# Performance work log

Hardware: AMD Instinct MI355X
Metric: run time of the kernel (lower is better)

The kernel has to match this reference:

```python
import jax, jax.numpy as jnp
import numpy as np

D_IN = 1024
D_OUT = 1024
NUM_HEADS = 16
D_HEAD = D_OUT // NUM_HEADS


def setup_inputs() -> dict:
    key = jax.random.key(0)
    ks = jax.random.split(key, 6)
    s = 0.02
    x = jax.random.normal(ks[0], (2, 2048, D_IN), dtype=jnp.float32)
    Wq = jax.random.normal(ks[1], (D_IN, D_OUT), dtype=jnp.float32) * s
    Wk = jax.random.normal(ks[2], (D_IN, D_OUT), dtype=jnp.float32) * s
    Wv = jax.random.normal(ks[3], (D_IN, D_OUT), dtype=jnp.float32) * s
    Wo = jax.random.normal(ks[4], (D_OUT, D_OUT), dtype=jnp.float32) * s
    bo = jnp.zeros((D_OUT,), dtype=jnp.float32)
    return {"x": x, "Wq": Wq, "Wk": Wk, "Wv": Wv, "Wo": Wo, "bo": bo}


def reference(x, Wq, Wk, Wv, Wo, bo):
    bs, S, _ = x.shape
    # QKV projections -> [b, h, s, d]
    def split_heads(t):
        return t.reshape(bs, S, NUM_HEADS, D_HEAD).transpose(0, 2, 1, 3)
    q = split_heads(x @ Wq)
    k = split_heads(x @ Wk)
    v = split_heads(x @ Wv)
    # scores [b, h, s, s], causal mask, scaled softmax
    scores = jnp.einsum("bhqd,bhkd->bhqk", q, k)
    causal = jnp.tril(jnp.ones((S, S), dtype=bool))
    scores = jnp.where(causal, scores, -jnp.inf)
    attn = jax.nn.softmax(scores / jnp.sqrt(jnp.float32(D_HEAD)), axis=-1)
    # dropout rate is 0.0 -> identity
    ctx = jnp.einsum("bhqk,bhkd->bhqd", attn, v)
    ctx = ctx.transpose(0, 2, 1, 3).reshape(bs, S, D_OUT)
    return ctx @ Wo + bo
```

## Files before the change

kernel.cpp:

```cpp
#include <hip/hip_runtime.h>
#include <math.h>

namespace {

constexpr int S   = 2048;
constexpr int D   = 1024;
constexpr int H   = 16;
constexpr int DH  = 64;
constexpr int B   = 2;
constexpr int M   = B * S;

typedef __attribute__((ext_vector_type(8)))  short bf16x8;
typedef __attribute__((ext_vector_type(4)))  float f32x4;
typedef __attribute__((ext_vector_type(16))) float f32x16;

__device__ __forceinline__ unsigned short f2bf(float f) {
    unsigned u = __builtin_bit_cast(unsigned, f);
    u += 0x7fffu + ((u >> 16) & 1u);
    return (unsigned short)(u >> 16);
}

__device__ __forceinline__ unsigned cvt_pk_bf16(float lo, float hi) {
    unsigned r;
    asm("v_cvt_pk_bf16_f32 %0, %1, %2" : "=v"(r) : "v"(lo), "v"(hi));
    return r;
}

__device__ __forceinline__ void gload16(const void* g, void* l) {
    __builtin_amdgcn_global_load_lds(
        (const __attribute__((address_space(1))) void*)g,
        (__attribute__((address_space(3))) void*)l, 16, 0, 0);
}

__global__ __launch_bounds__(256) void convert_x(
    const float* __restrict__ x, unsigned short* __restrict__ xb)
{
    const int i = (blockIdx.x * 256 + threadIdx.x) * 8;
    float4 a = *(const float4*)&x[i];
    float4 b = *(const float4*)&x[i + 4];
    ushort4 lo, hi;
    lo.x = f2bf(a.x); lo.y = f2bf(a.y); lo.z = f2bf(a.z); lo.w = f2bf(a.w);
    hi.x = f2bf(b.x); hi.y = f2bf(b.y); hi.z = f2bf(b.z); hi.w = f2bf(b.w);
    *(ushort4*)&xb[i]     = lo;
    *(ushort4*)&xb[i + 4] = hi;
}

__global__ __launch_bounds__(64) void convert_w(
    const float* __restrict__ Wq, const float* __restrict__ Wk,
    const float* __restrict__ Wv, const float* __restrict__ Wo,
    unsigned short* __restrict__ Wt)
{
    const int mat = blockIdx.z;
    const float* W = (mat == 0) ? Wq : (mat == 1) ? Wk : (mat == 2) ? Wv : Wo;
    const int n  = blockIdx.y * 64 + threadIdx.x;
    const int k0 = blockIdx.x * 8;
    ushort4 u0, u1;
    u0.x = f2bf(W[(size_t)(k0 + 0) * D + n]);
    u0.y = f2bf(W[(size_t)(k0 + 1) * D + n]);
    u0.z = f2bf(W[(size_t)(k0 + 2) * D + n]);
    u0.w = f2bf(W[(size_t)(k0 + 3) * D + n]);
    u1.x = f2bf(W[(size_t)(k0 + 4) * D + n]);
    u1.y = f2bf(W[(size_t)(k0 + 5) * D + n]);
    u1.z = f2bf(W[(size_t)(k0 + 6) * D + n]);
    u1.w = f2bf(W[(size_t)(k0 + 7) * D + n]);
    unsigned short* o = Wt + (size_t)mat * D * D + (size_t)n * D + k0;
    *(ushort4*)&o[0] = u0;
    *(ushort4*)&o[4] = u1;
}

__global__ __launch_bounds__(256) void gemm_qkv(
    const unsigned short* __restrict__ xb, const unsigned short* __restrict__ Wt,
    unsigned short* __restrict__ Qb, unsigned short* __restrict__ Kb,
    unsigned short* __restrict__ Vt)
{
    __shared__ unsigned short As[128 * 32];
    __shared__ unsigned short Bs[128 * 32];

    const int tid = threadIdx.x;
    const int l  = tid & 63;
    const int w  = tid >> 6;
    const int lr = l & 15;
    const int g  = l >> 4;
    const int wr = w >> 1, wc = w & 1;

    const int bm  = blockIdx.y;
    const int bnl = blockIdx.x;
    const int mat = bnl >> 3;
    const int n0  = (bnl & 7) * 128;
    const int m0  = bm * 128;
    const unsigned short* Bp = Wt + (size_t)mat * D * D;

    const int lrow = l >> 2;
    const int lcol = (l & 3) * 8;

    f32x4 acc[4][4];
    #pragma unroll
    for (int i = 0; i < 4; ++i)
        #pragma unroll
        for (int j = 0; j < 4; ++j) acc[i][j] = (f32x4){0.f, 0.f, 0.f, 0.f};

    for (int k0 = 0; k0 < D; k0 += 32) {
        #pragma unroll
        for (int p = 0; p < 2; ++p) {
            const int c = w * 2 + p;
            gload16(&xb[(size_t)(m0 + c * 16 + lrow) * D + k0 + lcol], &As[c * 512]);
            gload16(&Bp[(size_t)(n0 + c * 16 + lrow) * D + k0 + lcol], &Bs[c * 512]);
        }
        __syncthreads();
        bf16x8 af[4], bfr[4];
        #pragma unroll
        for (int i = 0; i < 4; ++i) {
            af[i]  = *(const bf16x8*)&As[(wr * 64 + i * 16 + lr) * 32 + g * 8];
            bfr[i] = *(const bf16x8*)&Bs[(wc * 64 + i * 16 + lr) * 32 + g * 8];
        }
        #pragma unroll
        for (int mi = 0; mi < 4; ++mi)
            #pragma unroll
            for (int ni = 0; ni < 4; ++ni)
                acc[mi][ni] = __builtin_amdgcn_mfma_f32_16x16x32_bf16(
                    af[mi], bfr[ni], acc[mi][ni], 0, 0, 0);
        __syncthreads();
    }

    const int b      = m0 >> 11;
    const int s_base = (m0 & (S - 1)) + wr * 64;
    if (mat == 2) {
        #pragma unroll
        for (int ni = 0; ni < 4; ++ni) {
            const int n  = n0 + wc * 64 + ni * 16 + lr;
            const int bh = b * H + (n >> 6);
            unsigned short* vp = Vt + ((size_t)bh * DH + (n & 63)) * S;
            #pragma unroll
            for (int mi = 0; mi < 4; ++mi) {
                const int s0 = s_base + mi * 16 + g * 4;
                ushort4 u;
                u.x = f2bf(acc[mi][ni][0]); u.y = f2bf(acc[mi][ni][1]);
                u.z = f2bf(acc[mi][ni][2]); u.w = f2bf(acc[mi][ni][3]);
                *(ushort4*)&vp[s0] = u;
            }
        }
    } else {
        unsigned short* Op = (mat == 0) ? Qb : Kb;
        #pragma unroll
        for (int mi = 0; mi < 4; ++mi)
            #pragma unroll
            for (int r = 0; r < 4; ++r) {
                const int s = s_base + mi * 16 + g * 4 + r;
                #pragma unroll
                for (int ni = 0; ni < 4; ++ni) {
                    const int n  = n0 + wc * 64 + ni * 16 + lr;
                    const int bh = b * H + (n >> 6);
                    Op[((size_t)bh * S + s) * DH + (n & 63)] = f2bf(acc[mi][ni][r]);
                }
            }
    }
}

__global__ __launch_bounds__(256) void gemm_out(
    const unsigned short* __restrict__ ctxb, const unsigned short* __restrict__ Wot,
    const float* __restrict__ bo, float* __restrict__ out)
{
    __shared__ unsigned short As[64 * 32];
    __shared__ unsigned short Bs[128 * 32];

    const int tid = threadIdx.x;
    const int l  = tid & 63;
    const int w  = tid >> 6;
    const int lr = l & 15;
    const int g  = l >> 4;
    const int wr = w >> 1, wc = w & 1;

    const int m0 = blockIdx.y * 64;
    const int n0 = blockIdx.x * 128;

    const int lrow = l >> 2;
    const int lcol = (l & 3) * 8;

    f32x4 acc[2][4];
    #pragma unroll
    for (int i = 0; i < 2; ++i)
        #pragma unroll
        for (int j = 0; j < 4; ++j) acc[i][j] = (f32x4){0.f, 0.f, 0.f, 0.f};

    for (int k0 = 0; k0 < D; k0 += 32) {
        gload16(&ctxb[(size_t)(m0 + w * 16 + lrow) * D + k0 + lcol], &As[w * 512]);
        #pragma unroll
        for (int p = 0; p < 2; ++p) {
            const int c = w * 2 + p;
            gload16(&Wot[(size_t)(n0 + c * 16 + lrow) * D + k0 + lcol], &Bs[c * 512]);
        }
        __syncthreads();
        bf16x8 af[2], bfr[4];
        #pragma unroll
        for (int i = 0; i < 2; ++i)
            af[i] = *(const bf16x8*)&As[(wr * 32 + i * 16 + lr) * 32 + g * 8];
        #pragma unroll
        for (int i = 0; i < 4; ++i)
            bfr[i] = *(const bf16x8*)&Bs[(wc * 64 + i * 16 + lr) * 32 + g * 8];
        #pragma unroll
        for (int mi = 0; mi < 2; ++mi)
            #pragma unroll
            for (int ni = 0; ni < 4; ++ni)
                acc[mi][ni] = __builtin_amdgcn_mfma_f32_16x16x32_bf16(
                    af[mi], bfr[ni], acc[mi][ni], 0, 0, 0);
        __syncthreads();
    }

    #pragma unroll
    for (int mi = 0; mi < 2; ++mi)
        #pragma unroll
        for (int ni = 0; ni < 4; ++ni) {
            const int n = n0 + wc * 64 + ni * 16 + lr;
            const float bias = bo[n];
            #pragma unroll
            for (int r = 0; r < 4; ++r) {
                const int m = m0 + wr * 32 + mi * 16 + g * 4 + r;
                out[(size_t)m * D + n] = acc[mi][ni][r] + bias;
            }
        }
}

__global__ __launch_bounds__(256, 2) void attn_mfma32(
    const unsigned short* __restrict__ Qb, const unsigned short* __restrict__ Kb,
    const unsigned short* __restrict__ Vt, unsigned short* __restrict__ ctxb)
{
    __shared__ unsigned short Ks[2][64 * 64];
    __shared__ unsigned short Vs[2][64 * 64];

    const int tid = threadIdx.x;
    const int l   = tid & 63;
    const int w   = tid >> 6;
    const int l31 = l & 31;
    const int hi  = l >> 5;

    const int lid = blockIdx.x;
    const int xcd = lid & 7;
    const int jj  = lid >> 3;
    const int bh  = xcd * 4 + (jj >> 4);
    const int qt  = 15 - (jj & 15);
    const int q0w = qt * 128 + w * 32;
    const int Fw  = q0w >> 6;
    const int NT  = 2 * qt + 2;

    const unsigned short* Qp = Qb + (size_t)bh * S * DH;
    const unsigned short* Kp = Kb + (size_t)bh * S * DH;
    const unsigned short* Vp = Vt + (size_t)bh * DH * S;

    bf16x8 qf[4];
    #pragma unroll
    for (int kk = 0; kk < 4; ++kk)
        qf[kk] = *(const bf16x8*)&Qp[(size_t)(q0w + l31) * DH + kk * 16 + hi * 8];

    f32x16 acc0 = {}, acc1 = {};
    float m = -1e30f, ll = 0.f;

    const int srow = l >> 3;
    const int ssw  = 8 * ((l & 7) ^ srow);

#define ATTN_STAGE(buf, t)                                                    \
    {                                                                         \
        const int kv0s = (t) * 64;                                            \
        _Pragma("unroll")                                                     \
        for (int p = 0; p < 2; ++p) {                                         \
            const int c   = w * 2 + p;                                        \
            const int row = c * 8 + srow;                                     \
            gload16(Kp + (size_t)(kv0s + row) * DH + ssw, &Ks[buf][c * 512]); \
            gload16(Vp + (size_t)row * S + kv0s + ssw, &Vs[buf][c * 512]);    \
        }                                                                     \
    }

    ATTN_STAGE(0, 0);
    __syncthreads();

    for (int t = 0; t < NT; ++t) {
        const int cur = t & 1;
        if (t + 1 < NT) ATTN_STAGE(cur ^ 1, t + 1);

        if (t <= Fw) {
            const int kv0  = t * 64;
            const bool diag = (t == Fw);

            f32x16 stl = {}, sth = {};
            #pragma unroll
            for (int kk = 0; kk < 4; ++kk) {
                const int cc = kk * 2 + hi;
                bf16x8 kl = *(const bf16x8*)&Ks[cur][l31 * 64 + ((cc ^ (l31 & 7)) * 8)];
                bf16x8 kh = *(const bf16x8*)&Ks[cur][(32 + l31) * 64 + ((cc ^ (l31 & 7)) * 8)];
                stl = __builtin_amdgcn_mfma_f32_32x32x16_bf16(kl, qf[kk], stl, 0, 0, 0);
                sth = __builtin_amdgcn_mfma_f32_32x32x16_bf16(kh, qf[kk], sth, 0, 0, 0);
            }

            const int qg = q0w + l31;
            float sc0[16], sc1[16];
            float pmax = -3e38f;
            #pragma unroll
            for (int r = 0; r < 16; ++r) {
                const int koff = (r & 3) + 8 * (r >> 2) + 4 * hi;
                float a = stl[r] * 0.125f;
                float b = sth[r] * 0.125f;
                if (diag) {
                    if (kv0 + koff > qg)      a = -3e38f;
                    if (kv0 + 32 + koff > qg) b = -3e38f;
                }
                sc0[r] = a; sc1[r] = b;
                pmax = fmaxf(pmax, fmaxf(a, b));
            }
            pmax = fmaxf(pmax, __shfl_xor(pmax, 32));

            if (!__all(pmax <= m + 8.f)) {
                const float newm = fmaxf(m, pmax);
                const float corr = __expf(m - newm);
                ll *= corr;
                #pragma unroll
                for (int r = 0; r < 16; ++r) { acc0[r] *= corr; acc1[r] *= corr; }
                m = newm;
            }
            float p0[16], p1[16], psum = 0.f;
            #pragma unroll
            for (int r = 0; r < 16; ++r) {
                p0[r] = __expf(sc0[r] - m); psum += p0[r];
                p1[r] = __expf(sc1[r] - m); psum += p1[r];
            }
            ll += psum + __shfl_xor(psum, 32);

            unsigned pw[16];
            #pragma unroll
            for (int tt = 0; tt < 8; ++tt) {
                pw[tt]     = cvt_pk_bf16(p0[2 * tt], p0[2 * tt + 1]);
                pw[8 + tt] = cvt_pk_bf16(p1[2 * tt], p1[2 * tt + 1]);
            }

            __builtin_amdgcn_s_setprio(1);
            #pragma unroll
            for (int ck = 0; ck < 4; ++ck) {
                const int t00 = 2 * ((2 * ck) & 3) + 8 * (ck >> 1);
                const int t10 = 2 * ((2 * ck + 1) & 3) + 8 * (ck >> 1);
                const unsigned sw0 = hi ? pw[t10]     : pw[t00];
                const unsigned sw1 = hi ? pw[t10 + 1] : pw[t00 + 1];
                const unsigned e0i = hi ? pw[t00]     : pw[t10];
                const unsigned e1i = hi ? pw[t00 + 1] : pw[t10 + 1];
                const unsigned e0  = __shfl_xor(e0i, 32);
                const unsigned e1  = __shfl_xor(e1i, 32);
                union { unsigned u[4]; bf16x8 v; } pb;
                pb.u[0] = hi ? e0  : sw0;
                pb.u[1] = hi ? e1  : sw1;
                pb.u[2] = hi ? sw0 : e0;
                pb.u[3] = hi ? sw1 : e1;
                const int cc = ck * 2 + hi;
                bf16x8 v0 = *(const bf16x8*)&Vs[cur][l31 * 64 + ((cc ^ (l31 & 7)) * 8)];
                bf16x8 v1 = *(const bf16x8*)&Vs[cur][(32 + l31) * 64 + ((cc ^ (l31 & 7)) * 8)];
                acc0 = __builtin_amdgcn_mfma_f32_32x32x16_bf16(v0, pb.v, acc0, 0, 0, 0);
                acc1 = __builtin_amdgcn_mfma_f32_32x32x16_bf16(v1, pb.v, acc1, 0, 0, 0);
            }
            __builtin_amdgcn_s_setprio(0);
        }
        __syncthreads();
    }

    const float inv = 1.f / ll;
    const int bb = bh >> 4, hh = bh & (H - 1);
    const int q  = q0w + l31;
    unsigned short* op = ctxb + ((size_t)(bb * S + q)) * D + hh * DH;
    #pragma unroll
    for (int t = 0; t < 8; ++t) {
        const int r0 = 2 * t;
        const int d  = (r0 & 3) + 8 * (r0 >> 2) + 4 * hi;
        *(unsigned*)&op[d]      = cvt_pk_bf16(acc0[r0] * inv, acc0[r0 + 1] * inv);
        *(unsigned*)&op[32 + d] = cvt_pk_bf16(acc1[r0] * inv, acc1[r0 + 1] * inv);
    }
#undef ATTN_STAGE
}

}

extern "C" void kernel_launch(void* const* d_in, const int* in_sizes, int n_in,
                              void* d_out, int out_size, void* d_ws, size_t ws_size,
                              hipStream_t stream) {
    const float* x  = (const float*)d_in[0];
    const float* Wq = (const float*)d_in[1];
    const float* Wk = (const float*)d_in[2];
    const float* Wv = (const float*)d_in[3];
    const float* Wo = (const float*)d_in[4];
    const float* bo = (const float*)d_in[5];
    float* out = (float*)d_out;

    unsigned short* xb   = (unsigned short*)d_ws;
    unsigned short* Wt   = xb + (size_t)M * D;
    unsigned short* Qb   = Wt + (size_t)4 * D * D;
    unsigned short* Kb   = Qb + (size_t)M * D;
    unsigned short* Vtp  = Kb + (size_t)M * D;
    unsigned short* ctxb = Vtp + (size_t)M * D;

    convert_x<<<dim3((M * D) / (256 * 8)), 256, 0, stream>>>(x, xb);
    convert_w<<<dim3(D / 8, D / 64, 4), 64, 0, stream>>>(Wq, Wk, Wv, Wo, Wt);
    gemm_qkv<<<dim3(24, M / 128), 256, 0, stream>>>(xb, Wt, Qb, Kb, Vtp);
    attn_mfma32<<<dim3(512), 256, 0, stream>>>(Qb, Kb, Vtp, ctxb);
    gemm_out<<<dim3(D / 128, M / 64), 256, 0, stream>>>(
        ctxb, Wt + (size_t)3 * D * D, bo, out);
}
```

Measured before the change: 226.7 us.

## Double-buffer LDS in projection GEMMs and rebalance attention block-to-tile mapping

Both projection GEMMs now use two LDS buffers, so the global-to-LDS load for the next K step is issued before the MFMA work on the current one, leaving one barrier per iteration instead of two. The attention kernel's block index mapping changes so the second round of heads walks query tiles in ascending order while the first walks them descending, pairing heavy and light causal tiles for better load balance. LDS use per GEMM block doubles, which may lower occupancy.

```diff
diff --git a/kernel.cpp b/kernel.cpp
--- a/kernel.cpp
+++ b/kernel.cpp
@@ -73,8 +73,8 @@
     unsigned short* __restrict__ Qb, unsigned short* __restrict__ Kb,
     unsigned short* __restrict__ Vt)
 {
-    __shared__ unsigned short As[128 * 32];
-    __shared__ unsigned short Bs[128 * 32];
+    __shared__ unsigned short As[2][128 * 32];
+    __shared__ unsigned short Bs[2][128 * 32];
 
     const int tid = threadIdx.x;
     const int l  = tid & 63;
@@ -99,19 +99,28 @@
         #pragma unroll
         for (int j = 0; j < 4; ++j) acc[i][j] = (f32x4){0.f, 0.f, 0.f, 0.f};
 
+#define QKV_STAGE(buf, kk0)                                                       \
+    {                                                                             \
+        _Pragma("unroll")                                                         \
+        for (int p = 0; p < 2; ++p) {                                             \
+            const int c = w * 2 + p;                                              \
+            gload16(&xb[(size_t)(m0 + c * 16 + lrow) * D + (kk0) + lcol],         \
+                    &As[buf][c * 512]);                                           \
+            gload16(&Bp[(size_t)(n0 + c * 16 + lrow) * D + (kk0) + lcol],         \
+                    &Bs[buf][c * 512]);                                           \
+        }                                                                         \
+    }
+
+    QKV_STAGE(0, 0);
+    __syncthreads();
+    int cur = 0;
     for (int k0 = 0; k0 < D; k0 += 32) {
-        #pragma unroll
-        for (int p = 0; p < 2; ++p) {
-            const int c = w * 2 + p;
-            gload16(&xb[(size_t)(m0 + c * 16 + lrow) * D + k0 + lcol], &As[c * 512]);
-            gload16(&Bp[(size_t)(n0 + c * 16 + lrow) * D + k0 + lcol], &Bs[c * 512]);
-        }
-        __syncthreads();
+        if (k0 + 32 < D) QKV_STAGE(cur ^ 1, k0 + 32);
         bf16x8 af[4], bfr[4];
         #pragma unroll
         for (int i = 0; i < 4; ++i) {
-            af[i]  = *(const bf16x8*)&As[(wr * 64 + i * 16 + lr) * 32 + g * 8];
-            bfr[i] = *(const bf16x8*)&Bs[(wc * 64 + i * 16 + lr) * 32 + g * 8];
+            af[i]  = *(const bf16x8*)&As[cur][(wr * 64 + i * 16 + lr) * 32 + g * 8];
+            bfr[i] = *(const bf16x8*)&Bs[cur][(wc * 64 + i * 16 + lr) * 32 + g * 8];
         }
         #pragma unroll
         for (int mi = 0; mi < 4; ++mi)
@@ -120,7 +129,9 @@
                 acc[mi][ni] = __builtin_amdgcn_mfma_f32_16x16x32_bf16(
                     af[mi], bfr[ni], acc[mi][ni], 0, 0, 0);
         __syncthreads();
-    }
+        cur ^= 1;
+    }
+#undef QKV_STAGE
 
     const int b      = m0 >> 11;
     const int s_base = (m0 & (S - 1)) + wr * 64;
@@ -160,8 +171,8 @@
     const unsigned short* __restrict__ ctxb, const unsigned short* __restrict__ Wot,
     const float* __restrict__ bo, float* __restrict__ out)
 {
-    __shared__ unsigned short As[64 * 32];
-    __shared__ unsigned short Bs[128 * 32];
+    __shared__ unsigned short As[2][64 * 32];
+    __shared__ unsigned short Bs[2][128 * 32];
 
     const int tid = threadIdx.x;
     const int l  = tid & 63;
@@ -182,21 +193,30 @@
         #pragma unroll
         for (int j = 0; j < 4; ++j) acc[i][j] = (f32x4){0.f, 0.f, 0.f, 0.f};
 
+#define OUT_STAGE(buf, kk0)                                                       \
+    {                                                                             \
+        gload16(&ctxb[(size_t)(m0 + w * 16 + lrow) * D + (kk0) + lcol],           \
+                &As[buf][w * 512]);                                               \
+        _Pragma("unroll")                                                         \
+        for (int p = 0; p < 2; ++p) {                                             \
+            const int c = w * 2 + p;                                              \
+            gload16(&Wot[(size_t)(n0 + c * 16 + lrow) * D + (kk0) + lcol],        \
+                    &Bs[buf][c * 512]);                                           \
+        }                                                                         \
+    }
+
+    OUT_STAGE(0, 0);
+    __syncthreads();
+    int cur = 0;
     for (int k0 = 0; k0 < D; k0 += 32) {
-        gload16(&ctxb[(size_t)(m0 + w * 16 + lrow) * D + k0 + lcol], &As[w * 512]);
-        #pragma unroll
-        for (int p = 0; p < 2; ++p) {
-            const int c = w * 2 + p;
-            gload16(&Wot[(size_t)(n0 + c * 16 + lrow) * D + k0 + lcol], &Bs[c * 512]);
-        }
-        __syncthreads();
+        if (k0 + 32 < D) OUT_STAGE(cur ^ 1, k0 + 32);
         bf16x8 af[2], bfr[4];
         #pragma unroll
         for (int i = 0; i < 2; ++i)
-            af[i] = *(const bf16x8*)&As[(wr * 32 + i * 16 + lr) * 32 + g * 8];
+            af[i] = *(const bf16x8*)&As[cur][(wr * 32 + i * 16 + lr) * 32 + g * 8];
         #pragma unroll
         for (int i = 0; i < 4; ++i)
-            bfr[i] = *(const bf16x8*)&Bs[(wc * 64 + i * 16 + lr) * 32 + g * 8];
+            bfr[i] = *(const bf16x8*)&Bs[cur][(wc * 64 + i * 16 + lr) * 32 + g * 8];
         #pragma unroll
         for (int mi = 0; mi < 2; ++mi)
             #pragma unroll
@@ -204,7 +224,9 @@
                 acc[mi][ni] = __builtin_amdgcn_mfma_f32_16x16x32_bf16(
                     af[mi], bfr[ni], acc[mi][ni], 0, 0, 0);
         __syncthreads();
-    }
+        cur ^= 1;
+    }
+#undef OUT_STAGE
 
     #pragma unroll
     for (int mi = 0; mi < 2; ++mi)
@@ -236,8 +258,12 @@
     const int lid = blockIdx.x;
     const int xcd = lid & 7;
     const int jj  = lid >> 3;
-    const int bh  = xcd * 4 + (jj >> 4);
-    const int qt  = 15 - (jj & 15);
+    const int rnd = jj >> 5;
+    const int pos = jj & 31;
+    const int sub = pos >> 4;
+    const int k16 = pos & 15;
+    const int bh  = xcd * 4 + rnd * 2 + sub;
+    const int qt  = rnd ? k16 : 15 - k16;
     const int q0w = qt * 128 + w * 32;
     const int Fw  = q0w >> 6;
     const int NT  = 2 * qt + 2;
```

Measured after the change: 241.8 us. +6.7%, slower.

## Double-buffer QKV GEMM LDS, unroll attention loop by two, rebalance causal tiles

Applied to the files above, without the earlier changes.

The QKV projection GEMM gains double-buffered LDS tiles so the global-to-LDS loads for the next K slice overlap the MFMA work on the current slice. The attention loop is manually unrolled by two with separate named K/V buffers, which makes buffer selection static. The attention block-to-tile mapping now alternates long-to-short and short-to-long causal query tiles across rounds to balance work per XCD. In exchange the GEMM uses twice the LDS, which may lower occupancy.

```diff
diff --git a/kernel.cpp b/kernel.cpp
--- a/kernel.cpp
+++ b/kernel.cpp
@@ -73,8 +73,10 @@
     unsigned short* __restrict__ Qb, unsigned short* __restrict__ Kb,
     unsigned short* __restrict__ Vt)
 {
-    __shared__ unsigned short As[128 * 32];
-    __shared__ unsigned short Bs[128 * 32];
+    __shared__ unsigned short As0[128 * 32];
+    __shared__ unsigned short As1[128 * 32];
+    __shared__ unsigned short Bs0[128 * 32];
+    __shared__ unsigned short Bs1[128 * 32];
 
     const int tid = threadIdx.x;
     const int l  = tid & 63;
@@ -99,28 +101,46 @@
         #pragma unroll
         for (int j = 0; j < 4; ++j) acc[i][j] = (f32x4){0.f, 0.f, 0.f, 0.f};
 
-    for (int k0 = 0; k0 < D; k0 += 32) {
-        #pragma unroll
-        for (int p = 0; p < 2; ++p) {
-            const int c = w * 2 + p;
-            gload16(&xb[(size_t)(m0 + c * 16 + lrow) * D + k0 + lcol], &As[c * 512]);
-            gload16(&Bp[(size_t)(n0 + c * 16 + lrow) * D + k0 + lcol], &Bs[c * 512]);
-        }
-        __syncthreads();
-        bf16x8 af[4], bfr[4];
-        #pragma unroll
-        for (int i = 0; i < 4; ++i) {
-            af[i]  = *(const bf16x8*)&As[(wr * 64 + i * 16 + lr) * 32 + g * 8];
-            bfr[i] = *(const bf16x8*)&Bs[(wc * 64 + i * 16 + lr) * 32 + g * 8];
-        }
-        #pragma unroll
-        for (int mi = 0; mi < 4; ++mi)
-            #pragma unroll
-            for (int ni = 0; ni < 4; ++ni)
-                acc[mi][ni] = __builtin_amdgcn_mfma_f32_16x16x32_bf16(
-                    af[mi], bfr[ni], acc[mi][ni], 0, 0, 0);
-        __syncthreads();
-    }
+#define QKV_STAGE(AD, BD, kk0)                                                    \
+    {                                                                             \
+        _Pragma("unroll")                                                         \
+        for (int p = 0; p < 2; ++p) {                                             \
+            const int c = w * 2 + p;                                              \
+            gload16(&xb[(size_t)(m0 + c * 16 + lrow) * D + (kk0) + lcol],         \
+                    &AD[c * 512]);                                                \
+            gload16(&Bp[(size_t)(n0 + c * 16 + lrow) * D + (kk0) + lcol],         \
+                    &BD[c * 512]);                                                \
+        }                                                                         \
+    }
+
+#define QKV_COMP(AS, BS)                                                          \
+    {                                                                             \
+        bf16x8 af[4], bfr[4];                                                     \
+        _Pragma("unroll")                                                         \
+        for (int i = 0; i < 4; ++i) {                                             \
+            af[i]  = *(const bf16x8*)&AS[(wr * 64 + i * 16 + lr) * 32 + g * 8];   \
+            bfr[i] = *(const bf16x8*)&BS[(wc * 64 + i * 16 + lr) * 32 + g * 8];   \
+        }                                                                         \
+        _Pragma("unroll")                                                         \
+        for (int mi = 0; mi < 4; ++mi)                                            \
+            _Pragma("unroll")                                                     \
+            for (int ni = 0; ni < 4; ++ni)                                        \
+                acc[mi][ni] = __builtin_amdgcn_mfma_f32_16x16x32_bf16(            \
+                    af[mi], bfr[ni], acc[mi][ni], 0, 0, 0);                       \
+    }
+
+    QKV_STAGE(As0, Bs0, 0);
+    __syncthreads();
+    for (int k0 = 0; k0 < D; k0 += 64) {
+        QKV_STAGE(As1, Bs1, k0 + 32);
+        QKV_COMP(As0, Bs0);
+        __syncthreads();
+        if (k0 + 64 < D) QKV_STAGE(As0, Bs0, k0 + 64);
+        QKV_COMP(As1, Bs1);
+        __syncthreads();
+    }
+#undef QKV_STAGE
+#undef QKV_COMP
 
     const int b      = m0 >> 11;
     const int s_base = (m0 & (S - 1)) + wr * 64;
@@ -224,8 +244,10 @@
     const unsigned short* __restrict__ Qb, const unsigned short* __restrict__ Kb,
     const unsigned short* __restrict__ Vt, unsigned short* __restrict__ ctxb)
 {
-    __shared__ unsigned short Ks[2][64 * 64];
-    __shared__ unsigned short Vs[2][64 * 64];
+    __shared__ unsigned short Ks0[64 * 64];
+    __shared__ unsigned short Ks1[64 * 64];
+    __shared__ unsigned short Vs0[64 * 64];
+    __shared__ unsigned short Vs1[64 * 64];
 
     const int tid = threadIdx.x;
     const int l   = tid & 63;
@@ -236,8 +258,12 @@
     const int lid = blockIdx.x;
     const int xcd = lid & 7;
     const int jj  = lid >> 3;
-    const int bh  = xcd * 4 + (jj >> 4);
-    const int qt  = 15 - (jj & 15);
+    const int rnd = jj >> 5;
+    const int pos = jj & 31;
+    const int sub = pos >> 4;
+    const int k16 = pos & 15;
+    const int bh  = xcd * 4 + rnd * 2 + sub;
+    const int qt  = rnd ? k16 : 15 - k16;
     const int q0w = qt * 128 + w * 32;
     const int Fw  = q0w >> 6;
     const int NT  = 2 * qt + 2;
@@ -257,105 +283,106 @@
     const int srow = l >> 3;
     const int ssw  = 8 * ((l & 7) ^ srow);
 
-#define ATTN_STAGE(buf, t)                                                    \
+#define ATTN_STAGE(KD, VD, t)                                                 \
     {                                                                         \
         const int kv0s = (t) * 64;                                            \
         _Pragma("unroll")                                                     \
         for (int p = 0; p < 2; ++p) {                                         \
             const int c   = w * 2 + p;                                        \
             const int row = c * 8 + srow;                                     \
-            gload16(Kp + (size_t)(kv0s + row) * DH + ssw, &Ks[buf][c * 512]); \
-            gload16(Vp + (size_t)row * S + kv0s + ssw, &Vs[buf][c * 512]);    \
-        }                                                                     \
-    }
-
-    ATTN_STAGE(0, 0);
+            gload16(Kp + (size_t)(kv0s + row) * DH + ssw, &KD[c * 512]);      \
+            gload16(Vp + (size_t)row * S + kv0s + ssw, &VD[c * 512]);         \
+        }                                                                     \
+    }
+
+#define ATTN_STEP(KSB, VSB, TT)                                               \
+    if ((TT) <= Fw) {                                                         \
+        const int kv0  = (TT) * 64;                                           \
+        const bool diag = ((TT) == Fw);                                       \
+        f32x16 stl = {}, sth = {};                                            \
+        _Pragma("unroll")                                                     \
+        for (int kk = 0; kk < 4; ++kk) {                                      \
+            const int cc = kk * 2 + hi;                                       \
+            bf16x8 kl = *(const bf16x8*)&KSB[l31 * 64 + ((cc ^ (l31 & 7)) * 8)]; \
+            bf16x8 kh = *(const bf16x8*)&KSB[(32 + l31) * 64 + ((cc ^ (l31 & 7)) * 8)]; \
+            stl = __builtin_amdgcn_mfma_f32_32x32x16_bf16(kl, qf[kk], stl, 0, 0, 0); \
+            sth = __builtin_amdgcn_mfma_f32_32x32x16_bf16(kh, qf[kk], sth, 0, 0, 0); \
+        }                                                                     \
+        const int qg = q0w + l31;                                             \
+        float sc0[16], sc1[16];                                               \
+        float pmax = -3e38f;                                                  \
+        _Pragma("unroll")                                                     \
+        for (int r = 0; r < 16; ++r) {                                        \
+            const int koff = (r & 3) + 8 * (r >> 2) + 4 * hi;                 \
+            float a = stl[r] * 0.125f;                                        \
+            float b2 = sth[r] * 0.125f;                                       \
+            if (diag) {                                                       \
+                if (kv0 + koff > qg)      a  = -3e38f;                        \
+                if (kv0 + 32 + koff > qg) b2 = -3e38f;                        \
+            }                                                                 \
+            sc0[r] = a; sc1[r] = b2;                                          \
+            pmax = fmaxf(pmax, fmaxf(a, b2));                                 \
+        }                                                                     \
+        pmax = fmaxf(pmax, __shfl_xor(pmax, 32));                             \
+        if (!__all(pmax <= m + 8.f)) {                                        \
+            const float newm = fmaxf(m, pmax);                                \
+            const float corr = __expf(m - newm);                              \
+            ll *= corr;                                                       \
+            _Pragma("unroll")                                                 \
+            for (int r = 0; r < 16; ++r) { acc0[r] *= corr; acc1[r] *= corr; }\
+            m = newm;                                                         \
+        }                                                                     \
+        float p0[16], p1[16], psum = 0.f;                                     \
+        _Pragma("unroll")                                                     \
+        for (int r = 0; r < 16; ++r) {                                        \
+            p0[r] = __expf(sc0[r] - m); psum += p0[r];                        \
+            p1[r] = __expf(sc1[r] - m); psum += p1[r];                        \
+        }                                                                     \
+        ll += psum + __shfl_xor(psum, 32);                                    \
+        unsigned pw[16];                                                      \
+        _Pragma("unroll")                                                     \
+        for (int tt = 0; tt < 8; ++tt) {                                      \
+            pw[tt]     = cvt_pk_bf16(p0[2 * tt], p0[2 * tt + 1]);             \
+            pw[8 + tt] = cvt_pk_bf16(p1[2 * tt], p1[2 * tt + 1]);             \
+        }                                                                     \
+        __builtin_amdgcn_s_setprio(1);                                        \
+        _Pragma("unroll")                                                     \
+        for (int ck = 0; ck < 4; ++ck) {                                      \
+            const int t00 = 2 * ((2 * ck) & 3) + 8 * (ck >> 1);               \
+            const int t10 = 2 * ((2 * ck + 1) & 3) + 8 * (ck >> 1);           \
+            const unsigned sw0 = hi ? pw[t10]     : pw[t00];                  \
+            const unsigned sw1 = hi ? pw[t10 + 1] : pw[t00 + 1];              \
+            const unsigned e0i = hi ? pw[t00]     : pw[t10];                  \
+            const unsigned e1i = hi ? pw[t00 + 1] : pw[t10 + 1];              \
+            const unsigned e0  = __shfl_xor(e0i, 32);                         \
+            const unsigned e1  = __shfl_xor(e1i, 32);                         \
+            union { unsigned u[4]; bf16x8 v; } pb;                            \
+            pb.u[0] = hi ? e0  : sw0;                                         \
+            pb.u[1] = hi ? e1  : sw1;                                         \
+            pb.u[2] = hi ? sw0 : e0;                                          \
+            pb.u[3] = hi ? sw1 : e1;                                          \
+            const int cc = ck * 2 + hi;                                       \
+            bf16x8 v0 = *(const bf16x8*)&VSB[l31 * 64 + ((cc ^ (l31 & 7)) * 8)]; \
+            bf16x8 v1 = *(const bf16x8*)&VSB[(32 + l31) * 64 + ((cc ^ (l31 & 7)) * 8)]; \
+            acc0 = __builtin_amdgcn_mfma_f32_32x32x16_bf16(v0, pb.v, acc0, 0, 0, 0); \
+            acc1 = __builtin_amdgcn_mfma_f32_32x32x16_bf16(v1, pb.v, acc1, 0, 0, 0); \
+        }                                                                     \
+        __builtin_amdgcn_s_setprio(0);                                        \
+    }
+
+    ATTN_STAGE(Ks0, Vs0, 0);
     __syncthreads();
 
-    for (int t = 0; t < NT; ++t) {
-        const int cur = t & 1;
-        if (t + 1 < NT) ATTN_STAGE(cur ^ 1, t + 1);
-
-        if (t <= Fw) {
-            const int kv0  = t * 64;
-            const bool diag = (t == Fw);
-
-            f32x16 stl = {}, sth = {};
-            #pragma unroll
-            for (int kk = 0; kk < 4; ++kk) {
-                const int cc = kk * 2 + hi;
-                bf16x8 kl = *(const bf16x8*)&Ks[cur][l31 * 64 + ((cc ^ (l31 & 7)) * 8)];
-                bf16x8 kh = *(const bf16x8*)&Ks[cur][(32 + l31) * 64 + ((cc ^ (l31 & 7)) * 8)];
-                stl = __builtin_amdgcn_mfma_f32_32x32x16_bf16(kl, qf[kk], stl, 0, 0, 0);
-                sth = __builtin_amdgcn_mfma_f32_32x32x16_bf16(kh, qf[kk], sth, 0, 0, 0);
-            }
-
-            const int qg = q0w + l31;
-            float sc0[16], sc1[16];
-            float pmax = -3e38f;
-            #pragma unroll
-            for (int r = 0; r < 16; ++r) {
-                const int koff = (r & 3) + 8 * (r >> 2) + 4 * hi;
-                float a = stl[r] * 0.125f;
-                float b = sth[r] * 0.125f;
-                if (diag) {
-                    if (kv0 + koff > qg)      a = -3e38f;
-                    if (kv0 + 32 + koff > qg) b = -3e38f;
-                }
-                sc0[r] = a; sc1[r] = b;
-                pmax = fmaxf(pmax, fmaxf(a, b));
-            }
-            pmax = fmaxf(pmax, __shfl_xor(pmax, 32));
-
-            if (!__all(pmax <= m + 8.f)) {
-                const float newm = fmaxf(m, pmax);
-                const float corr = __expf(m - newm);
-                ll *= corr;
-                #pragma unroll
-                for (int r = 0; r < 16; ++r) { acc0[r] *= corr; acc1[r] *= corr; }
-                m = newm;
-            }
-            float p0[16], p1[16], psum = 0.f;
-            #pragma unroll
-            for (int r = 0; r < 16; ++r) {
-                p0[r] = __expf(sc0[r] - m); psum += p0[r];
-                p1[r] = __expf(sc1[r] - m); psum += p1[r];
-            }
-            ll += psum + __shfl_xor(psum, 32);
-
-            unsigned pw[16];
-            #pragma unroll
-            for (int tt = 0; tt < 8; ++tt) {
-                pw[tt]     = cvt_pk_bf16(p0[2 * tt], p0[2 * tt + 1]);
-                pw[8 + tt] = cvt_pk_bf16(p1[2 * tt], p1[2 * tt + 1]);
-            }
-
-            __builtin_amdgcn_s_setprio(1);
-            #pragma unroll
-            for (int ck = 0; ck < 4; ++ck) {
-                const int t00 = 2 * ((2 * ck) & 3) + 8 * (ck >> 1);
-                const int t10 = 2 * ((2 * ck + 1) & 3) + 8 * (ck >> 1);
-                const unsigned sw0 = hi ? pw[t10]     : pw[t00];
-                const unsigned sw1 = hi ? pw[t10 + 1] : pw[t00 + 1];
-                const unsigned e0i = hi ? pw[t00]     : pw[t10];
-                const unsigned e1i = hi ? pw[t00 + 1] : pw[t10 + 1];
-                const unsigned e0  = __shfl_xor(e0i, 32);
-                const unsigned e1  = __shfl_xor(e1i, 32);
-                union { unsigned u[4]; bf16x8 v; } pb;
-                pb.u[0] = hi ? e0  : sw0;
-                pb.u[1] = hi ? e1  : sw1;
-                pb.u[2] = hi ? sw0 : e0;
-                pb.u[3] = hi ? sw1 : e1;
-                const int cc = ck * 2 + hi;
-                bf16x8 v0 = *(const bf16x8*)&Vs[cur][l31 * 64 + ((cc ^ (l31 & 7)) * 8)];
-                bf16x8 v1 = *(const bf16x8*)&Vs[cur][(32 + l31) * 64 + ((cc ^ (l31 & 7)) * 8)];
-                acc0 = __builtin_amdgcn_mfma_f32_32x32x16_bf16(v0, pb.v, acc0, 0, 0, 0);
-                acc1 = __builtin_amdgcn_mfma_f32_32x32x16_bf16(v1, pb.v, acc1, 0, 0, 0);
-            }
-            __builtin_amdgcn_s_setprio(0);
-        }
-        __syncthreads();
-    }
+    for (int t = 0; t < NT; t += 2) {
+        ATTN_STAGE(Ks1, Vs1, t + 1);
+        ATTN_STEP(Ks0, Vs0, t);
+        __syncthreads();
+        if (t + 2 < NT) ATTN_STAGE(Ks0, Vs0, t + 2);
+        ATTN_STEP(Ks1, Vs1, t + 1);
+        __syncthreads();
+    }
+#undef ATTN_STAGE
+#undef ATTN_STEP
 
     const float inv = 1.f / ll;
     const int bb = bh >> 4, hh = bh & (H - 1);
@@ -368,7 +395,6 @@
         *(unsigned*)&op[d]      = cvt_pk_bf16(acc0[r0] * inv, acc0[r0 + 1] * inv);
         *(unsigned*)&op[32 + d] = cvt_pk_bf16(acc1[r0] * inv, acc1[r0 + 1] * inv);
     }
-#undef ATTN_STAGE
 }
 
 }
```

Result: faster. 205.6 us (-9.3%).
